# Performance work log

Measured on AMD Instinct MI355X. Metric: run time of the kernel, lower is better.

Reference implementation:

```python
import jax, jax.numpy as jnp
import numpy as np

N_NODES = 100000
N_EDGES = 400000
F_IN = 128
HEADS = 4
C1 = 64   # conv1 out per head
C2 = 128  # conv2 out per head
G = 2048  # num graphs
FP = 2048
HID = 64
NEG_SLOPE = 0.2


def _gat_conv(x, edge_index, W, a_src, a_dst, b, heads, ch):
    """PyG-style GATConv with self-loops, concat=True."""
    n = x.shape[0]
    loops = jnp.arange(n, dtype=edge_index.dtype)
    src = jnp.concatenate([edge_index[0], loops])
    dst = jnp.concatenate([edge_index[1], loops])
    h = (x @ W).reshape(n, heads, ch)                      # [N,H,C]
    e_src = jnp.sum(h * a_src, axis=-1)                    # [N,H]
    e_dst = jnp.sum(h * a_dst, axis=-1)                    # [N,H]
    logits = jax.nn.leaky_relu(e_src[src] + e_dst[dst], NEG_SLOPE)  # [E,H]
    m = jax.ops.segment_max(logits, dst, num_segments=n)   # per-dst max
    p = jnp.exp(logits - m[dst])
    denom = jax.ops.segment_sum(p, dst, num_segments=n)
    alpha = p / denom[dst]                                 # [E,H]
    out = jax.ops.segment_sum(h[src] * alpha[:, :, None], dst, num_segments=n)
    return out.reshape(n, heads * ch) + b


def setup_inputs() -> dict:
    key = jax.random.key(0)
    ks = jax.random.split(key, 16)
    s = 0.05
    inp = {
        "x": jax.random.normal(ks[0], (N_NODES, F_IN), jnp.float32),
        "edge_index": jax.random.randint(ks[1], (2, N_EDGES), 0, N_NODES, jnp.int32),
        "batch": jnp.sort(jax.random.randint(ks[2], (N_NODES,), 0, G, jnp.int32)),
        "fp": jax.random.normal(ks[3], (G, FP), jnp.float32),
        "W1": jax.random.normal(ks[4], (F_IN, HEADS * C1), jnp.float32) * s,
        "a_src1": jax.random.normal(ks[5], (HEADS, C1), jnp.float32) * s,
        "a_dst1": jax.random.normal(ks[6], (HEADS, C1), jnp.float32) * s,
        "b1": jnp.zeros((HEADS * C1,), jnp.float32),
        "W2": jax.random.normal(ks[7], (HEADS * C1, HEADS * C2), jnp.float32) * s,
        "a_src2": jax.random.normal(ks[8], (HEADS, C2), jnp.float32) * s,
        "a_dst2": jax.random.normal(ks[9], (HEADS, C2), jnp.float32) * s,
        "b2": jnp.zeros((HEADS * C2,), jnp.float32),
        "Wfp": jax.random.normal(ks[10], (FP, HID), jnp.float32) * s,
        "bfp": jnp.zeros((HID,), jnp.float32),
        "Wfc1": jax.random.normal(ks[11], (HEADS * C2 + HID, HID), jnp.float32) * s,
        "bfc1": jnp.zeros((HID,), jnp.float32),
        "Wfc2": jax.random.normal(ks[12], (HID, 1), jnp.float32) * s,
        "bfc2": jnp.zeros((1,), jnp.float32),
    }
    return inp


def reference(x, edge_index, batch, fp, W1, a_src1, a_dst1, b1, W2, a_src2, a_dst2, b2,
              Wfp, bfp, Wfc1, bfc1, Wfc2, bfc2):
    h = _gat_conv(x, edge_index, W1, a_src1, a_dst1, b1, HEADS, C1)
    h = jax.nn.elu(h)
    h = _gat_conv(h, edge_index, W2, a_src2, a_dst2, b2, HEADS, C2)
    h = jax.nn.elu(h)
    # global mean pool over graphs
    sums = jax.ops.segment_sum(h, batch, num_segments=G)
    counts = jax.ops.segment_sum(jnp.ones((h.shape[0], 1), h.dtype), batch, num_segments=G)
    pooled = sums / jnp.maximum(counts, 1.0)               # [G, 512]
    fph = fp @ Wfp + bfp                                   # [G, 64]
    z = jnp.concatenate([pooled, fph], axis=1)             # [G, 576]
    z = jax.nn.relu(z @ Wfc1 + bfc1)
    # dropout is identity in eval mode
    return z @ Wfc2 + bfc2                                 # [G, 1]
```

## Files before the change

### kernel.cpp

```cpp
#include <hip/hip_runtime.h>
#include <math.h>

#define NEG_SLOPE 0.2f

typedef __attribute__((ext_vector_type(8))) short bf16x8;
typedef __attribute__((ext_vector_type(4))) float f32x4;
typedef __attribute__((ext_vector_type(2))) float f32x2;

__device__ __forceinline__ float b2f(short s) {
  return __uint_as_float(((unsigned int)(unsigned short)s) << 16);
}
__device__ __forceinline__ unsigned short f2b_rne(float f) {
  unsigned int u = __float_as_uint(f);
  u = (u + 0x7FFF + ((u >> 16) & 1)) >> 16;
  return (unsigned short)u;
}

__device__ __forceinline__ void fp8x8_to_f32(uint2 raw, float* f) {
  f32x2 a = __builtin_amdgcn_cvt_pk_f32_fp8((int)raw.x, false);
  f32x2 b = __builtin_amdgcn_cvt_pk_f32_fp8((int)raw.x, true);
  f32x2 c = __builtin_amdgcn_cvt_pk_f32_fp8((int)raw.y, false);
  f32x2 d = __builtin_amdgcn_cvt_pk_f32_fp8((int)raw.y, true);
  f[0] = a[0]; f[1] = a[1]; f[2] = b[0]; f[3] = b[1];
  f[4] = c[0]; f[5] = c[1]; f[6] = d[0]; f[7] = d[1];
}

__device__ __forceinline__ void gload16(const unsigned short* g, unsigned short* l) {
  __builtin_amdgcn_global_load_lds(
      (const __attribute__((address_space(1))) unsigned int*)g,
      (__attribute__((address_space(3))) unsigned int*)l, 16, 0, 0);
}

template<int N> __device__ __forceinline__ void vmwait() {
  asm volatile("s_waitcnt vmcnt(%0)" :: "n"(N) : "memory");
}

__device__ __forceinline__ void tr_one(const float* __restrict__ W,
                                       unsigned short* __restrict__ WT,
                                       int K, int N, int idx)
{
  if (idx < K * N) {
    int k = idx / N, n = idx - k * N;
    WT[(size_t)n * K + k] = f2b_rne(W[idx]);
  }
}

__global__ __launch_bounds__(256) void prep_all(
    const float* __restrict__ x, unsigned short* __restrict__ xb, size_t nx, int B0,
    const float* __restrict__ fp, unsigned short* __restrict__ fpb, size_t nf, int B1,
    const float* __restrict__ W1, unsigned short* __restrict__ W1T,
    const float* __restrict__ W2, unsigned short* __restrict__ W2T,
    const float* __restrict__ Wfp, unsigned short* __restrict__ WfpT,
    const float* __restrict__ Wfc1, unsigned short* __restrict__ Wfc1T)
{
  int b = blockIdx.x;
  const int t = threadIdx.x;
  if (b < B0) {
    size_t i = (size_t)b * 256 + t;
    if (i < nx) xb[i] = f2b_rne(x[i]);
    return;
  }
  b -= B0;
  if (b < B1) {
    size_t i = (size_t)b * 256 + t;
    if (i < nf) fpb[i] = f2b_rne(fp[i]);
    return;
  }
  b -= B1;
  if (b < 128) { tr_one(W1, W1T, 128, 256, b * 256 + t); return; }
  b -= 128;
  if (b < 512) { tr_one(W2, W2T, 256, 512, b * 256 + t); return; }
  b -= 512;
  if (b < 512) { tr_one(Wfp, WfpT, 2048, 64, b * 256 + t); return; }
  b -= 512;
  tr_one(Wfc1, Wfc1T, 576, 64, b * 256 + t);
}

template<int EMODE, int KK>
__global__ __launch_bounds__(256) void gemm_mfma(
    const unsigned short* __restrict__ A, const unsigned short* __restrict__ BT,
    unsigned char* __restrict__ Cout, int M, int N,
    const float* __restrict__ a_src, const float* __restrict__ a_dst,
    float* __restrict__ es, float* __restrict__ ed, int nh)
{
  constexpr int NT = KK / 32;
  __shared__ unsigned short As[4][128 * 32];
  __shared__ unsigned short Bs[4][128 * 32];
  const int tid  = threadIdx.x;
  const int wave = tid >> 6;
  const int lane = tid & 63;
  const int ln   = lane & 15;
  const int quad = lane >> 4;
  const int wr0  = (wave >> 1) * 64;
  const int wc0  = (wave & 1) * 64;

  const int nwg = gridDim.x;
  const int ncol = N >> 7;
  const int bid = blockIdx.x;
  const int qq = nwg >> 3, rr = nwg & 7;
  const int xc = bid & 7, io = bid >> 3;
  const int swz = (xc < rr ? xc * (qq + 1) : rr * (qq + 1) + (xc - rr) * qq) + io;
  const int bn = (swz % ncol) * 128;
  const int bm = (swz / ncol) * 128;

  const int srow = lane >> 2;
  const int cch  = lane & 3;
  const int rt0  = wave * 32 + srow;
  const int ksw  = ((cch ^ (srow & 3)) << 3);
  int ar0 = bm + rt0;      if (ar0 >= M) ar0 = M - 1;
  int ar1 = bm + rt0 + 16; if (ar1 >= M) ar1 = M - 1;
  const unsigned short* gA0 = A + (size_t)ar0 * KK + ksw;
  const unsigned short* gA1 = A + (size_t)ar1 * KK + ksw;
  const unsigned short* gB0 = BT + (size_t)(bn + rt0) * KK + ksw;
  const unsigned short* gB1 = BT + (size_t)(bn + rt0 + 16) * KK + ksw;

  auto stage = [&](int T) {
    const int b = T & 3;
    const int kk = T * 32;
    gload16(gA0 + kk, &As[b][(wave * 32) * 32]);
    gload16(gA1 + kk, &As[b][(wave * 32 + 16) * 32]);
    gload16(gB0 + kk, &Bs[b][(wave * 32) * 32]);
    gload16(gB1 + kk, &Bs[b][(wave * 32 + 16) * 32]);
  };

  f32x4 acc[4][4];
  const f32x4 z4 = {0.f, 0.f, 0.f, 0.f};
#pragma unroll
  for (int i = 0; i < 4; ++i)
#pragma unroll
    for (int j = 0; j < 4; ++j) acc[i][j] = z4;

  stage(0); stage(1); stage(2);

#pragma unroll
  for (int t = 0; t < NT; ++t) {
    if (t + 3 < NT) stage(t + 3);
    if      (t < NT - 3) vmwait<12>();
    else if (t == NT - 3) vmwait<8>();
    else if (t == NT - 2) vmwait<4>();
    else                  vmwait<0>();
    __builtin_amdgcn_s_barrier();
    __builtin_amdgcn_sched_barrier(0);
    const int b = t & 3;
    bf16x8 af[4], bfv[4];
#pragma unroll
    for (int i = 0; i < 4; ++i) {
      const int row = wr0 + i * 16 + ln;
      af[i] = *(const bf16x8*)(&As[b][row * 32 + ((quad ^ (ln & 3)) << 3)]);
    }
#pragma unroll
    for (int j = 0; j < 4; ++j) {
      const int row = wc0 + j * 16 + ln;
      bfv[j] = *(const bf16x8*)(&Bs[b][row * 32 + ((quad ^ (ln & 3)) << 3)]);
    }
#pragma unroll
    for (int i = 0; i < 4; ++i)
#pragma unroll
      for (int j = 0; j < 4; ++j)
        acc[i][j] = __builtin_amdgcn_mfma_f32_16x16x32_bf16(af[i], bfv[j], acc[i][j], 0, 0, 0);
    __builtin_amdgcn_sched_barrier(0);
    __builtin_amdgcn_s_barrier();
  }

#pragma unroll
  for (int i = 0; i < 4; ++i) {
#pragma unroll
    for (int r = 0; r < 4; ++r) {
      int row = bm + wr0 + i * 16 + quad * 4 + r;
      if (row >= M) continue;
      int p01 = __builtin_amdgcn_cvt_pk_fp8_f32(acc[i][0][r], acc[i][1][r], 0, false);
      int p23 = __builtin_amdgcn_cvt_pk_fp8_f32(acc[i][2][r], acc[i][3][r], 0, false);
      size_t rb = (size_t)row * N + bn + wc0 + ln;
      Cout[rb +  0] = (unsigned char)(p01 & 0xff);
      Cout[rb + 16] = (unsigned char)((p01 >> 8) & 0xff);
      Cout[rb + 32] = (unsigned char)(p23 & 0xff);
      Cout[rb + 48] = (unsigned char)((p23 >> 8) & 0xff);
    }
  }

  float asv[4], adv[4];
#pragma unroll
  for (int j = 0; j < 4; ++j) {
    int col = bn + wc0 + j * 16 + ln;
    asv[j] = a_src[col];
    adv[j] = a_dst[col];
  }
  if (EMODE == 64) {
    const int head = (bn + wc0) >> 6;
#pragma unroll
    for (int i = 0; i < 4; ++i) {
#pragma unroll
      for (int r = 0; r < 4; ++r) {
        float ps = 0.f, pd = 0.f;
#pragma unroll
        for (int j = 0; j < 4; ++j) {
          ps = fmaf(acc[i][j][r], asv[j], ps);
          pd = fmaf(acc[i][j][r], adv[j], pd);
        }
        for (int off = 8; off; off >>= 1) {
          ps += __shfl_down(ps, off, 16);
          pd += __shfl_down(pd, off, 16);
        }
        if (ln == 0) {
          int row = bm + wr0 + i * 16 + quad * 4 + r;
          if (row < M) {
            es[(size_t)row * nh + head] = ps;
            ed[(size_t)row * nh + head] = pd;
          }
        }
      }
    }
  } else {
    float* esp = (float*)As[0];
    float* edp = esp + 256;
#pragma unroll
    for (int i = 0; i < 4; ++i) {
#pragma unroll
      for (int r = 0; r < 4; ++r) {
        float ps = 0.f, pd = 0.f;
#pragma unroll
        for (int j = 0; j < 4; ++j) {
          ps = fmaf(acc[i][j][r], asv[j], ps);
          pd = fmaf(acc[i][j][r], adv[j], pd);
        }
        for (int off = 8; off; off >>= 1) {
          ps += __shfl_down(ps, off, 16);
          pd += __shfl_down(pd, off, 16);
        }
        if (ln == 0) {
          int rl = wr0 + i * 16 + quad * 4 + r;
          esp[rl * 2 + (wc0 >> 6)] = ps;
          edp[rl * 2 + (wc0 >> 6)] = pd;
        }
      }
    }
    __syncthreads();
    if (tid < 128) {
      int row = bm + tid;
      if (row < M) {
        int head = bn >> 7;
        es[(size_t)row * nh + head] = esp[tid * 2] + esp[tid * 2 + 1];
        ed[(size_t)row * nh + head] = edp[tid * 2] + edp[tid * 2 + 1];
      }
    }
  }
}

__global__ __launch_bounds__(256) void gemm_mfma_n64(
    const unsigned short* __restrict__ A, int lda,
    const unsigned short* __restrict__ BT, int ldb,
    float* __restrict__ Cp, int M, int kchunk)
{
  const int LDT = 72;
  __shared__ unsigned short As[128 * 72];
  __shared__ unsigned short Bs[64 * 72];
  const int tid  = threadIdx.x;
  const int wave = tid >> 6;
  const int lane = tid & 63;
  const int ln   = lane & 15;
  const int quad = lane >> 4;
  const int ks   = blockIdx.x;
  const int bm   = blockIdx.y * 128;
  const int k_beg = ks * kchunk;
  const int k_end = k_beg + kchunk;
  const int arow = tid >> 1;
  const int akb  = (tid & 1) * 32;
  const int brow = tid >> 2;
  const int bkb  = (tid & 3) * 16;

  f32x4 acc[2][4];
  const f32x4 z4 = {0.f, 0.f, 0.f, 0.f};
#pragma unroll
  for (int i = 0; i < 2; ++i)
#pragma unroll
    for (int j = 0; j < 4; ++j) acc[i][j] = z4;

  for (int k0 = k_beg; k0 < k_end; k0 += 64) {
    const unsigned short* ap = A + (size_t)(bm + arow) * lda + k0 + akb;
#pragma unroll
    for (int q = 0; q < 4; ++q)
      *(bf16x8*)(&As[arow * LDT + akb + q * 8]) = *(const bf16x8*)(ap + q * 8);
    const unsigned short* bp = BT + (size_t)brow * ldb + k0 + bkb;
#pragma unroll
    for (int q = 0; q < 2; ++q)
      *(bf16x8*)(&Bs[brow * LDT + bkb + q * 8]) = *(const bf16x8*)(bp + q * 8);
    __syncthreads();
#pragma unroll
    for (int kk = 0; kk < 2; ++kk) {
      bf16x8 af[2], bfv[4];
#pragma unroll
      for (int i = 0; i < 2; ++i)
        af[i] = *(const bf16x8*)(&As[(wave * 32 + i * 16 + ln) * LDT + kk * 32 + quad * 8]);
#pragma unroll
      for (int j = 0; j < 4; ++j)
        bfv[j] = *(const bf16x8*)(&Bs[(j * 16 + ln) * LDT + kk * 32 + quad * 8]);
#pragma unroll
      for (int i = 0; i < 2; ++i)
#pragma unroll
        for (int j = 0; j < 4; ++j)
          acc[i][j] = __builtin_amdgcn_mfma_f32_16x16x32_bf16(af[i], bfv[j], acc[i][j], 0, 0, 0);
    }
    __syncthreads();
  }
#pragma unroll
  for (int i = 0; i < 2; ++i)
#pragma unroll
    for (int r = 0; r < 4; ++r) {
      int row = bm + wave * 32 + i * 16 + quad * 4 + r;
#pragma unroll
      for (int j = 0; j < 4; ++j)
        Cp[((size_t)ks * M + row) * 64 + j * 16 + ln] = acc[i][j][r];
    }
}

__global__ void fp_finish(const float* __restrict__ Cp, int ksplit, int M,
                          const float* __restrict__ bfp,
                          unsigned short* __restrict__ zb)
{
  const int g = blockIdx.x;
  const int j = threadIdx.x;
  float s = bfp[j];
  for (int ks = 0; ks < ksplit; ++ks) s += Cp[((size_t)ks * M + g) * 64 + j];
  zb[(size_t)g * 576 + 512 + j] = f2b_rne(s);
}

__global__ void mlp_finish(const float* __restrict__ Cp, int ksplit, int M,
                           const float* __restrict__ bfc1,
                           const float* __restrict__ Wfc2, const float* __restrict__ bfc2,
                           float* __restrict__ out)
{
  const int g = blockIdx.x;
  const int j = threadIdx.x;
  float s = bfc1[j];
  for (int ks = 0; ks < ksplit; ++ks) s += Cp[((size_t)ks * M + g) * 64 + j];
  s = s > 0.f ? s : 0.f;
  float term = s * Wfc2[j];
  for (int off = 32; off; off >>= 1) term += __shfl_down(term, off, 64);
  if (j == 0) out[g] = term + bfc2[0];
}

__global__ void count_all(const int* __restrict__ ei, int E, int* __restrict__ deg,
                          const int* __restrict__ batch, int NN, int* __restrict__ gcnt,
                          int BE)
{
  int b = blockIdx.x;
  int t = threadIdx.x;
  if (b < BE) {
    int e = b * 256 + t;
    if (e < E) atomicAdd(&deg[ei[E + e]], 1);
  } else {
    int i = (b - BE) * 256 + t;
    if (i < NN) atomicAdd(&gcnt[batch[i]], 1);
  }
}

__global__ void fill_csr(const int* __restrict__ ei, int E, int* __restrict__ cursor,
                         const int* __restrict__ rowptr, int* __restrict__ csr_src)
{
  int e = blockIdx.x * 256 + threadIdx.x;
  if (e < E) {
    int d = ei[E + e];
    int pos = atomicAdd(&cursor[d], 1);
    csr_src[rowptr[d] + pos] = ei[e];
  }
}

__device__ void scan_p1_body(const int* __restrict__ vals, int n, int* __restrict__ bsum,
                             int bb)
{
  __shared__ int red[256];
  int base = bb * 1024;
  int t = threadIdx.x;
  int s = 0;
#pragma unroll
  for (int i = 0; i < 4; ++i) {
    int idx = base + i * 256 + t;
    if (idx < n) s += vals[idx];
  }
  red[t] = s;
  __syncthreads();
  for (int off = 128; off; off >>= 1) {
    if (t < off) red[t] += red[t + off];
    __syncthreads();
  }
  if (t == 0) bsum[bb] = red[0];
}

__global__ void scan2_p1(const int* __restrict__ vA, int nA, int* __restrict__ bsA, int nbA,
                         const int* __restrict__ vB, int nB, int* __restrict__ bsB)
{
  int b = blockIdx.x;
  if (b < nbA) scan_p1_body(vA, nA, bsA, b);
  else         scan_p1_body(vB, nB, bsB, b - nbA);
}

__device__ void scan_p2_body(const int* __restrict__ bsum, int* __restrict__ bpre,
                             int nb, int* __restrict__ rowptr, int n)
{
  __shared__ int tmp[128];
  int t = threadIdx.x;
  int v = (t < nb) ? bsum[t] : 0;
  tmp[t] = v;
  __syncthreads();
  for (int off = 1; off < 128; off <<= 1) {
    int add = (t >= off) ? tmp[t - off] : 0;
    __syncthreads();
    tmp[t] += add;
    __syncthreads();
  }
  if (t < nb) bpre[t] = tmp[t] - v;
  if (t == 127) rowptr[n] = tmp[127];
}

__global__ void scan2_p2(const int* __restrict__ bsA, int* __restrict__ bpA, int nbA,
                         int* __restrict__ rpA, int nA,
                         const int* __restrict__ bsB, int* __restrict__ bpB, int nbB,
                         int* __restrict__ rpB, int nB)
{
  if (blockIdx.x == 0) scan_p2_body(bsA, bpA, nbA, rpA, nA);
  else                 scan_p2_body(bsB, bpB, nbB, rpB, nB);
}

__device__ void scan_p3_body(const int* __restrict__ vals, const int* __restrict__ bpre,
                             int n, int* __restrict__ rowptr, int bb)
{
  __shared__ int tmp[256];
  int t = threadIdx.x;
  int base = bb * 1024 + t * 4;
  int v[4]; int s = 0;
#pragma unroll
  for (int i = 0; i < 4; ++i) {
    int idx = base + i;
    v[i] = (idx < n) ? vals[idx] : 0;
    s += v[i];
  }
  tmp[t] = s;
  __syncthreads();
  for (int off = 1; off < 256; off <<= 1) {
    int add = (t >= off) ? tmp[t - off] : 0;
    __syncthreads();
    tmp[t] += add;
    __syncthreads();
  }
  int run = bpre[bb] + tmp[t] - s;
#pragma unroll
  for (int i = 0; i < 4; ++i) {
    int idx = base + i;
    if (idx < n) rowptr[idx] = run;
    run += v[i];
  }
}

__global__ void scan2_p3(const int* __restrict__ vA, const int* __restrict__ bpA, int nA,
                         int* __restrict__ rpA, int nbA,
                         const int* __restrict__ vB, const int* __restrict__ bpB, int nB,
                         int* __restrict__ rpB)
{
  int b = blockIdx.x;
  if (b < nbA) scan_p3_body(vA, bpA, nA, rpA, b);
  else         scan_p3_body(vB, bpB, nB, rpB, b - nbA);
}

__global__ void alpha_kernel(const float* __restrict__ es, const float* __restrict__ ed,
                             const int* __restrict__ rowptr, const int* __restrict__ csr_src,
                             float* __restrict__ w_csr, float* __restrict__ wself,
                             float* __restrict__ dinv, int N, int nh)
{
  int idx = blockIdx.x * 256 + threadIdx.x;
  if (idx >= N * nh) return;
  const int dst = idx / nh;
  const int h = idx - dst * nh;
  const float edh = ed[(size_t)dst * nh + h];
  const int beg = rowptr[dst], end = rowptr[dst + 1];
  float sum = 0.f;
  for (int e = beg; e < end; ++e) {
    int s = csr_src[e];
    float l = es[(size_t)s * nh + h] + edh;
    l = l >= 0.f ? l : NEG_SLOPE * l;
    float w = expf(l);
    w_csr[(size_t)e * nh + h] = w;
    sum += w;
  }
  float ls = es[(size_t)dst * nh + h] + edh;
  ls = ls >= 0.f ? ls : NEG_SLOPE * ls;
  float wsl = expf(ls);
  sum += wsl;
  wself[(size_t)dst * nh + h] = wsl;
  dinv[(size_t)dst * nh + h] = 1.0f / sum;
}

__global__ __launch_bounds__(256) void aggregate_b(
    const unsigned char* __restrict__ h,
    const float* __restrict__ w_csr, const float* __restrict__ wself,
    const float* __restrict__ dinv,
    const int* __restrict__ rowptr, const int* __restrict__ csr_src,
    const float* __restrict__ bias, unsigned short* __restrict__ out,
    int N, int nh, int C)
{
  const int HC = nh * C;
  const int CH8 = HC >> 3;
  const int dpb = 256 / CH8;
  const int grp = threadIdx.x / CH8;
  const int lane = threadIdx.x - grp * CH8;
  const int dst = blockIdx.x * dpb + grp;
  if (dst >= N) return;
  const int ch = lane << 3;
  const int head = ch / C;
  const int beg = rowptr[dst], end = rowptr[dst + 1];
  float acc[8] = {0.f, 0.f, 0.f, 0.f, 0.f, 0.f, 0.f, 0.f};
  float hv[8];
  int e = beg;
  for (; e + 1 < end; e += 2) {
    int s0 = csr_src[e], s1 = csr_src[e + 1];
    float a0 = w_csr[(size_t)e * nh + head];
    float a1 = w_csr[(size_t)(e + 1) * nh + head];
    uint2 r0 = *(const uint2*)(h + (size_t)s0 * HC + ch);
    uint2 r1 = *(const uint2*)(h + (size_t)s1 * HC + ch);
    fp8x8_to_f32(r0, hv);
#pragma unroll
    for (int r = 0; r < 8; ++r) acc[r] = fmaf(a0, hv[r], acc[r]);
    fp8x8_to_f32(r1, hv);
#pragma unroll
    for (int r = 0; r < 8; ++r) acc[r] = fmaf(a1, hv[r], acc[r]);
  }
  if (e < end) {
    int s0 = csr_src[e];
    float a0 = w_csr[(size_t)e * nh + head];
    uint2 r0 = *(const uint2*)(h + (size_t)s0 * HC + ch);
    fp8x8_to_f32(r0, hv);
#pragma unroll
    for (int r = 0; r < 8; ++r) acc[r] = fmaf(a0, hv[r], acc[r]);
  }
  {
    float a = wself[(size_t)dst * nh + head];
    uint2 r0 = *(const uint2*)(h + (size_t)dst * HC + ch);
    fp8x8_to_f32(r0, hv);
#pragma unroll
    for (int r = 0; r < 8; ++r) acc[r] = fmaf(a, hv[r], acc[r]);
  }
  const float di = dinv[(size_t)dst * nh + head];
  bf16x8 o;
#pragma unroll
  for (int r = 0; r < 8; ++r) {
    float v = acc[r] * di + bias[ch + r];
    v = v > 0.f ? v : (expf(v) - 1.0f);
    o[r] = (short)f2b_rne(v);
  }
  *(bf16x8*)(out + (size_t)dst * HC + ch) = o;
}

__global__ __launch_bounds__(256) void agg_pool(
    const unsigned char* __restrict__ h,
    const float* __restrict__ w_csr, const float* __restrict__ wself,
    const float* __restrict__ dinv,
    const int* __restrict__ rowptr, const int* __restrict__ csr_src,
    const float* __restrict__ bias, const int* __restrict__ grp,
    unsigned short* __restrict__ zb)
{
  const int g = blockIdx.x;
  const int wave = threadIdx.x >> 6;
  const int lane = threadIdx.x & 63;
  const int ch = lane << 3;
  const int head = lane >> 4;
  const int gbeg = grp[g], gend = grp[g + 1];
  float bch[8];
#pragma unroll
  for (int r = 0; r < 8; ++r) bch[r] = bias[ch + r];
  float pool[8] = {0.f, 0.f, 0.f, 0.f, 0.f, 0.f, 0.f, 0.f};
  float hv[8];

  for (int node = gbeg + wave; node < gend; node += 4) {
    const int beg = rowptr[node], end = rowptr[node + 1];
    float acc[8] = {0.f, 0.f, 0.f, 0.f, 0.f, 0.f, 0.f, 0.f};
    int e = beg;
    for (; e + 1 < end; e += 2) {
      int s0 = csr_src[e], s1 = csr_src[e + 1];
      float a0 = w_csr[(size_t)e * 4 + head];
      float a1 = w_csr[(size_t)(e + 1) * 4 + head];
      uint2 r0 = *(const uint2*)(h + (size_t)s0 * 512 + ch);
      uint2 r1 = *(const uint2*)(h + (size_t)s1 * 512 + ch);
      fp8x8_to_f32(r0, hv);
#pragma unroll
      for (int r = 0; r < 8; ++r) acc[r] = fmaf(a0, hv[r], acc[r]);
      fp8x8_to_f32(r1, hv);
#pragma unroll
      for (int r = 0; r < 8; ++r) acc[r] = fmaf(a1, hv[r], acc[r]);
    }
    if (e < end) {
      int s0 = csr_src[e];
      float a0 = w_csr[(size_t)e * 4 + head];
      uint2 r0 = *(const uint2*)(h + (size_t)s0 * 512 + ch);
      fp8x8_to_f32(r0, hv);
#pragma unroll
      for (int r = 0; r < 8; ++r) acc[r] = fmaf(a0, hv[r], acc[r]);
    }
    {
      float a = wself[(size_t)node * 4 + head];
      uint2 r0 = *(const uint2*)(h + (size_t)node * 512 + ch);
      fp8x8_to_f32(r0, hv);
#pragma unroll
      for (int r = 0; r < 8; ++r) acc[r] = fmaf(a, hv[r], acc[r]);
    }
    const float di = dinv[(size_t)node * 4 + head];
#pragma unroll
    for (int r = 0; r < 8; ++r) {
      float v = acc[r] * di + bch[r];
      v = v > 0.f ? v : (expf(v) - 1.0f);
      pool[r] += v;
    }
  }

  __shared__ float red[4][512];
#pragma unroll
  for (int r = 0; r < 8; ++r) red[wave][ch + r] = pool[r];
  __syncthreads();
  const float inv = 1.0f / (float)max(gend - gbeg, 1);
#pragma unroll
  for (int k = 0; k < 2; ++k) {
    int c = threadIdx.x + k * 256;
    float s = (red[0][c] + red[1][c]) + (red[2][c] + red[3][c]);
    zb[(size_t)g * 576 + c] = f2b_rne(s * inv);
  }
}

extern "C" void kernel_launch(void* const* d_in, const int* in_sizes, int n_in,
                              void* d_out, int out_size, void* d_ws, size_t ws_size,
                              hipStream_t stream)
{
  const float* x      = (const float*)d_in[0];
  const int*   ei     = (const int*)d_in[1];
  const int*   batch  = (const int*)d_in[2];
  const float* fp     = (const float*)d_in[3];
  const float* W1     = (const float*)d_in[4];
  const float* a_src1 = (const float*)d_in[5];
  const float* a_dst1 = (const float*)d_in[6];
  const float* b1     = (const float*)d_in[7];
  const float* W2     = (const float*)d_in[8];
  const float* a_src2 = (const float*)d_in[9];
  const float* a_dst2 = (const float*)d_in[10];
  const float* b2     = (const float*)d_in[11];
  const float* Wfp    = (const float*)d_in[12];
  const float* bfp    = (const float*)d_in[13];
  const float* Wfc1   = (const float*)d_in[14];
  const float* bfc1   = (const float*)d_in[15];
  const float* Wfc2   = (const float*)d_in[16];
  const float* bfc2   = (const float*)d_in[17];
  float* out = (float*)d_out;

  const int NN = in_sizes[0] / 128;
  const int E  = in_sizes[1] / 2;
  const int G  = in_sizes[3] / 2048;
  const int FIN = 128, H = 4, C1 = 64, C2 = 128;
  const int HC1 = H * C1;
  const int HC2 = H * C2;
  const int KFP = in_sizes[3] / G;
  const int KZ  = HC2 + 64;
  const int KS_FP = 16;
  const int KS_Z  = 9;

  char* base = (char*)d_ws;
  size_t off = 0;
  auto alloc = [&](size_t bytes) {
    char* p = base + off; off += (bytes + 255) & ~(size_t)255; return p;
  };
  size_t xb_sz  = ((size_t)NN * FIN * 2 + 255) & ~(size_t)255;
  size_t h1b_sz = (size_t)NN * HC1;
  size_t h2b_sz = (size_t)NN * HC2;
  size_t rA = xb_sz + h1b_sz; if (h2b_sz > rA) rA = h2b_sz;
  char* RA = alloc(rA);
  unsigned short* xb  = (unsigned short*)RA;
  unsigned char*  h1b = (unsigned char*)(RA + xb_sz);
  unsigned char*  h2b = (unsigned char*)RA;
  size_t fpb_sz  = ((size_t)G * KFP * 2 + 255) & ~(size_t)255;
  size_t cpfp_sz = (size_t)KS_FP * G * 64 * 4;
  size_t agg1_sz = (size_t)NN * HC1 * 2;
  size_t rB = fpb_sz + cpfp_sz; if (agg1_sz > rB) rB = agg1_sz;
  char* RB = alloc(rB);
  unsigned short* fpb   = (unsigned short*)RB;
  float*          Cp_fp = (float*)(RB + fpb_sz);
  unsigned short* agg1b = (unsigned short*)RB;
  float* w1     = (float*)alloc((size_t)E * H * 4);
  float* wself1 = (float*)alloc((size_t)NN * H * 4);
  float* es1    = (float*)alloc((size_t)NN * H * 4);
  float* ed1    = (float*)alloc((size_t)NN * H * 4);
  float* dinv1  = (float*)alloc((size_t)NN * H * 4);
  float* w2 = w1, *wself2 = wself1, *es2 = es1, *ed2 = ed1, *dinv2 = dinv1;
  unsigned short* zb    = (unsigned short*)alloc((size_t)G * KZ * 2);
  float*          Cp_z  = (float*)alloc((size_t)KS_Z * G * 64 * 4);
  unsigned short* W1T   = (unsigned short*)alloc((size_t)HC1 * FIN * 2);
  unsigned short* W2T   = (unsigned short*)alloc((size_t)HC2 * HC1 * 2);
  unsigned short* WfpT  = (unsigned short*)alloc((size_t)64 * KFP * 2);
  unsigned short* Wfc1T = (unsigned short*)alloc((size_t)64 * KZ * 2);
  int* iarena   = (int*)alloc(((size_t)2 * NN + G) * 4);
  int* deg      = iarena;
  int* cursor   = iarena + NN;
  int* gcnt     = iarena + 2 * NN;
  int* rowptr_n = (int*)alloc(((size_t)NN + 1) * 4);
  int* rowptr_g = (int*)alloc(((size_t)G + 1) * 4);
  int* csr_src  = (int*)alloc((size_t)E * 4);
  int* bsumA    = (int*)alloc(128 * 4);
  int* bpreA    = (int*)alloc(128 * 4);
  int* bsumB    = (int*)alloc(128 * 4);
  int* bpreB    = (int*)alloc(128 * 4);

  const size_t nx = (size_t)NN * FIN;
  const size_t nf = (size_t)G * KFP;
  const int B0 = (int)((nx + 255) / 256);
  const int B1 = (int)((nf + 255) / 256);
  {
    int nb = B0 + B1 + 128 + 512 + 512 + 144;
    prep_all<<<nb, 256, 0, stream>>>(x, xb, nx, B0, fp, fpb, nf, B1,
                                     W1, W1T, W2, W2T, Wfp, WfpT, Wfc1, Wfc1T);
  }

  {
    dim3 gg(KS_FP, G / 128);
    gemm_mfma_n64<<<gg, 256, 0, stream>>>(fpb, KFP, WfpT, KFP, Cp_fp, G, KFP / KS_FP);
    fp_finish<<<G, 64, 0, stream>>>(Cp_fp, KS_FP, G, bfp, zb);
  }

  hipMemsetAsync(iarena, 0, sizeof(int) * ((size_t)2 * NN + G), stream);
  {
    int BE = (E + 255) / 256;
    int BN = (NN + 255) / 256;
    count_all<<<BE + BN, 256, 0, stream>>>(ei, E, deg, batch, NN, gcnt, BE);
  }
  {
    int nbA = (NN + 1023) / 1024;
    int nbB = (G + 1023) / 1024;
    scan2_p1<<<nbA + nbB, 256, 0, stream>>>(deg, NN, bsumA, nbA, gcnt, G, bsumB);
    scan2_p2<<<2, 128, 0, stream>>>(bsumA, bpreA, nbA, rowptr_n, NN,
                                    bsumB, bpreB, nbB, rowptr_g, G);
    scan2_p3<<<nbA + nbB, 256, 0, stream>>>(deg, bpreA, NN, rowptr_n, nbA,
                                            gcnt, bpreB, G, rowptr_g);
  }
  fill_csr<<<(E + 255) / 256, 256, 0, stream>>>(ei, E, cursor, rowptr_n, csr_src);

  {
    const int nrow = (NN + 127) / 128;
    gemm_mfma<64, 128><<<nrow * (HC1 / 128), 256, 0, stream>>>(
        xb, W1T, h1b, NN, HC1, a_src1, a_dst1, es1, ed1, H);
  }
  alpha_kernel<<<(NN * H + 255) / 256, 256, 0, stream>>>(es1, ed1, rowptr_n, csr_src,
                                                         w1, wself1, dinv1, NN, H);
  aggregate_b<<<(NN + 7) / 8, 256, 0, stream>>>(h1b, w1, wself1, dinv1, rowptr_n, csr_src,
                                                b1, agg1b, NN, H, C1);

  {
    const int nrow = (NN + 127) / 128;
    gemm_mfma<128, 256><<<nrow * (HC2 / 128), 256, 0, stream>>>(
        agg1b, W2T, h2b, NN, HC2, a_src2, a_dst2, es2, ed2, H);
  }
  alpha_kernel<<<(NN * H + 255) / 256, 256, 0, stream>>>(es2, ed2, rowptr_n, csr_src,
                                                         w2, wself2, dinv2, NN, H);
  agg_pool<<<G, 256, 0, stream>>>(h2b, w2, wself2, dinv2, rowptr_n, csr_src,
                                  b2, rowptr_g, zb);

  {
    dim3 gg(KS_Z, G / 128);
    gemm_mfma_n64<<<gg, 256, 0, stream>>>(zb, KZ, Wfc1T, KZ, Cp_z, G, KZ / KS_Z);
    mlp_finish<<<G, 64, 0, stream>>>(Cp_z, KS_Z, G, bfc1, Wfc2, bfc2, out);
  }
}
```

Baseline: 461.6 us.

## Stage fp8 GEMM output through LDS for coalesced stores; use 3-stage pipeline

The GEMM epilogue now packs each row's four fp8 values into one 32-bit LDS word. The tile is then transposed through shared memory so that each thread writes 16-byte coalesced global stores, replacing the scattered single-byte stores. The K-loop prefetch pipeline drops from 4 to 3 LDS buffers, issues the next stage after the barrier, and removes the trailing barrier per iteration. This cuts LDS footprint and barrier count. In exchange it adds an extra LDS round-trip and a sync in the epilogue.

New measurement: 464.1 us. No clear change (+0.5%).

```diff
diff --git a/kernel.cpp b/kernel.cpp
--- a/kernel.cpp
+++ b/kernel.cpp
@@ -33,6 +33,11 @@
 
 template<int N> __device__ __forceinline__ void vmwait() {
   asm volatile("s_waitcnt vmcnt(%0)" :: "n"(N) : "memory");
+}
+
+__device__ __forceinline__ unsigned int bsel(uint4 d, int s) {
+  return ((d.x >> (8 * s)) & 0xffu) | (((d.y >> (8 * s)) & 0xffu) << 8)
+       | (((d.z >> (8 * s)) & 0xffu) << 16) | (((d.w >> (8 * s)) & 0xffu) << 24);
 }
 
 __device__ __forceinline__ void tr_one(const float* __restrict__ W,
@@ -84,8 +89,8 @@
     float* __restrict__ es, float* __restrict__ ed, int nh)
 {
   constexpr int NT = KK / 32;
-  __shared__ unsigned short As[4][128 * 32];
-  __shared__ unsigned short Bs[4][128 * 32];
+  __shared__ unsigned short As[3][128 * 32];
+  __shared__ unsigned short Bs[3][128 * 32];
   const int tid  = threadIdx.x;
   const int wave = tid >> 6;
   const int lane = tid & 63;
@@ -115,7 +120,7 @@
   const unsigned short* gB1 = BT + (size_t)(bn + rt0 + 16) * KK + ksw;
 
   auto stage = [&](int T) {
-    const int b = T & 3;
+    const int b = T % 3;
     const int kk = T * 32;
     gload16(gA0 + kk, &As[b][(wave * 32) * 32]);
     gload16(gA1 + kk, &As[b][(wave * 32 + 16) * 32]);
@@ -130,18 +135,15 @@
 #pragma unroll
     for (int j = 0; j < 4; ++j) acc[i][j] = z4;
 
-  stage(0); stage(1); stage(2);
+  stage(0); stage(1);
 
 #pragma unroll
   for (int t = 0; t < NT; ++t) {
-    if (t + 3 < NT) stage(t + 3);
-    if      (t < NT - 3) vmwait<12>();
-    else if (t == NT - 3) vmwait<8>();
-    else if (t == NT - 2) vmwait<4>();
-    else                  vmwait<0>();
+    if (t < NT - 1) vmwait<4>(); else vmwait<0>();
     __builtin_amdgcn_s_barrier();
     __builtin_amdgcn_sched_barrier(0);
-    const int b = t & 3;
+    if (t + 2 < NT) stage(t + 2);
+    const int b = t % 3;
     bf16x8 af[4], bfv[4];
 #pragma unroll
     for (int i = 0; i < 4; ++i) {
@@ -158,23 +160,19 @@
 #pragma unroll
       for (int j = 0; j < 4; ++j)
         acc[i][j] = __builtin_amdgcn_mfma_f32_16x16x32_bf16(af[i], bfv[j], acc[i][j], 0, 0, 0);
-    __builtin_amdgcn_sched_barrier(0);
-    __builtin_amdgcn_s_barrier();
-  }
-
+  }
+  __syncthreads();
+
+  unsigned int* Cb = (unsigned int*)As;
+  const int cbase = (wc0 >> 2) + ln;
 #pragma unroll
   for (int i = 0; i < 4; ++i) {
 #pragma unroll
     for (int r = 0; r < 4; ++r) {
-      int row = bm + wr0 + i * 16 + quad * 4 + r;
-      if (row >= M) continue;
-      int p01 = __builtin_amdgcn_cvt_pk_fp8_f32(acc[i][0][r], acc[i][1][r], 0, false);
-      int p23 = __builtin_amdgcn_cvt_pk_fp8_f32(acc[i][2][r], acc[i][3][r], 0, false);
-      size_t rb = (size_t)row * N + bn + wc0 + ln;
-      Cout[rb +  0] = (unsigned char)(p01 & 0xff);
-      Cout[rb + 16] = (unsigned char)((p01 >> 8) & 0xff);
-      Cout[rb + 32] = (unsigned char)(p23 & 0xff);
-      Cout[rb + 48] = (unsigned char)((p23 >> 8) & 0xff);
+      int rowl = wr0 + i * 16 + quad * 4 + r;
+      int p = __builtin_amdgcn_cvt_pk_fp8_f32(acc[i][0][r], acc[i][1][r], 0, false);
+      p     = __builtin_amdgcn_cvt_pk_fp8_f32(acc[i][2][r], acc[i][3][r], p, true);
+      Cb[rowl * 36 + cbase] = (unsigned int)p;
     }
   }
 
@@ -185,63 +183,68 @@
     asv[j] = a_src[col];
     adv[j] = a_dst[col];
   }
-  if (EMODE == 64) {
-    const int head = (bn + wc0) >> 6;
-#pragma unroll
-    for (int i = 0; i < 4; ++i) {
-#pragma unroll
-      for (int r = 0; r < 4; ++r) {
-        float ps = 0.f, pd = 0.f;
-#pragma unroll
-        for (int j = 0; j < 4; ++j) {
-          ps = fmaf(acc[i][j][r], asv[j], ps);
-          pd = fmaf(acc[i][j][r], adv[j], pd);
-        }
-        for (int off = 8; off; off >>= 1) {
-          ps += __shfl_down(ps, off, 16);
-          pd += __shfl_down(pd, off, 16);
-        }
-        if (ln == 0) {
-          int row = bm + wr0 + i * 16 + quad * 4 + r;
+  float* esp = (float*)Bs;
+  float* edp = esp + 256;
+#pragma unroll
+  for (int i = 0; i < 4; ++i) {
+#pragma unroll
+    for (int r = 0; r < 4; ++r) {
+      float ps = 0.f, pd = 0.f;
+#pragma unroll
+      for (int j = 0; j < 4; ++j) {
+        ps = fmaf(acc[i][j][r], asv[j], ps);
+        pd = fmaf(acc[i][j][r], adv[j], pd);
+      }
+      for (int off = 8; off; off >>= 1) {
+        ps += __shfl_down(ps, off, 16);
+        pd += __shfl_down(pd, off, 16);
+      }
+      if (ln == 0) {
+        int rl = wr0 + i * 16 + quad * 4 + r;
+        if (EMODE == 64) {
+          int row = bm + rl;
           if (row < M) {
+            int head = (bn + wc0) >> 6;
             es[(size_t)row * nh + head] = ps;
             ed[(size_t)row * nh + head] = pd;
           }
-        }
-      }
-    }
-  } else {
-    float* esp = (float*)As[0];
-    float* edp = esp + 256;
-#pragma unroll
-    for (int i = 0; i < 4; ++i) {
-#pragma unroll
-      for (int r = 0; r < 4; ++r) {
-        float ps = 0.f, pd = 0.f;
-#pragma unroll
-        for (int j = 0; j < 4; ++j) {
-          ps = fmaf(acc[i][j][r], asv[j], ps);
-          pd = fmaf(acc[i][j][r], adv[j], pd);
-        }
-        for (int off = 8; off; off >>= 1) {
-          ps += __shfl_down(ps, off, 16);
-          pd += __shfl_down(pd, off, 16);
-        }
-        if (ln == 0) {
-          int rl = wr0 + i * 16 + quad * 4 + r;
+        } else {
           esp[rl * 2 + (wc0 >> 6)] = ps;
           edp[rl * 2 + (wc0 >> 6)] = pd;
         }
       }
     }
-    __syncthreads();
-    if (tid < 128) {
-      int row = bm + tid;
-      if (row < M) {
-        int head = bn >> 7;
-        es[(size_t)row * nh + head] = esp[tid * 2] + esp[tid * 2 + 1];
-        ed[(size_t)row * nh + head] = edp[tid * 2] + edp[tid * 2 + 1];
-      }
+  }
+  __syncthreads();
+
+  {
+    const int rT = tid >> 1;
+    const int hT = tid & 1;
+    const unsigned int* cp = &Cb[rT * 36 + 16 * hT];
+    uint4 d0 = *(const uint4*)(cp + 0);
+    uint4 d1 = *(const uint4*)(cp + 4);
+    uint4 d2 = *(const uint4*)(cp + 8);
+    uint4 d3 = *(const uint4*)(cp + 12);
+    int grow = bm + rT;
+    if (grow < M) {
+      unsigned char* gp = Cout + (size_t)grow * N + bn + 64 * hT;
+      uint4 o;
+      o.x = bsel(d0, 0); o.y = bsel(d1, 0); o.z = bsel(d2, 0); o.w = bsel(d3, 0);
+      *(uint4*)(gp + 0) = o;
+      o.x = bsel(d0, 1); o.y = bsel(d1, 1); o.z = bsel(d2, 1); o.w = bsel(d3, 1);
+      *(uint4*)(gp + 16) = o;
+      o.x = bsel(d0, 2); o.y = bsel(d1, 2); o.z = bsel(d2, 2); o.w = bsel(d3, 2);
+      *(uint4*)(gp + 32) = o;
+      o.x = bsel(d0, 3); o.y = bsel(d1, 3); o.z = bsel(d2, 3); o.w = bsel(d3, 3);
+      *(uint4*)(gp + 48) = o;
+    }
+  }
+  if (EMODE == 128 && tid < 128) {
+    int row = bm + tid;
+    if (row < M) {
+      int head = bn >> 7;
+      es[(size_t)row * nh + head] = esp[tid * 2] + esp[tid * 2 + 1];
+      ed[(size_t)row * nh + head] = edp[tid * 2] + edp[tid * 2 + 1];
     }
   }
 }
```
